# Kernel tuning notes

Hardware: AMD Instinct MI355X
Metric: run time of the kernel (lower is better)

Reference implementation:

```python
import jax, jax.numpy as jnp
import numpy as np

B, D, H, C, V, SAMPLE_NUM = 4096, 1024, 512, 50, 4, 10000


def ds_combin_two(alpha1, alpha2, K):
    """Dempster-Shafer combination of two Dirichlet parameter sets [B, K]."""
    S1 = jnp.sum(alpha1, axis=1, keepdims=True)
    S2 = jnp.sum(alpha2, axis=1, keepdims=True)
    b1 = (alpha1 - 1.0) / S1
    b2 = (alpha2 - 1.0) / S2
    u1 = K / S1  # [B,1]
    u2 = K / S2
    # bb_sum - bb_diag computed without materializing [B,K,K] outer product:
    # sum_ij b1_i b2_j = sum(b1)*sum(b2); diag sum = sum_i b1_i b2_i
    Cconf = jnp.sum(b1, axis=1) * jnp.sum(b2, axis=1) - jnp.sum(b1 * b2, axis=1)  # [B]
    denom = (1.0 - Cconf)[:, None]
    b_a = (b1 * b2 + b1 * u2 + b2 * u1) / denom
    u_a = (u1 * u2) / denom  # [B,1]
    S_a = K / u_a
    e_a = b_a * S_a
    return e_a + 1.0


def setup_inputs() -> dict:
    key = jax.random.key(0)
    ks = jax.random.split(key, 8)
    x = jax.random.normal(ks[0], (V, B, D), dtype=jnp.float32)
    indexes = jax.random.randint(ks[1], (B,), 0, SAMPLE_NUM)
    W1 = jax.random.normal(ks[2], (V, D, H), dtype=jnp.float32) * (1.0 / np.sqrt(D))
    b1 = jax.random.normal(ks[3], (V, H), dtype=jnp.float32) * 0.01
    W2 = jax.random.normal(ks[4], (V, H, C), dtype=jnp.float32) * (1.0 / np.sqrt(H))
    b2 = jax.random.normal(ks[5], (V, C), dtype=jnp.float32) * 0.01
    # original init: identity per (view, sample); add small noise so the
    eye = jnp.eye(C, dtype=jnp.float32)
    matrixes = eye[None, None] + 0.01 * jax.random.normal(ks[6], (V, SAMPLE_NUM, C, C), dtype=jnp.float32)
    return {"x": x, "indexes": indexes, "W1": W1, "b1": b1, "W2": W2, "b2": b2, "matrixes": matrixes}


def reference(x, indexes, W1, b1, W2, b2, matrixes):
    K = W2.shape[-1]
    n_views = x.shape[0]
    # per-view classifier MLP: Linear->ReLU->Linear->Softplus
    h = jax.nn.relu(jnp.einsum("vbd,vdh->vbh", x, W1) + b1[:, None, :])
    evidence = jax.nn.softplus(jnp.einsum("vbh,vhc->vbc", h, W2) + b2[:, None, :])  # [V,B,C]
    # transferByMatrix (training path): per-sample gathered [C,C] matmul
    sel = matrixes[:, indexes]  # [V,B,C,C]
    transferred = jnp.einsum("vbc,vbcd->vbd", evidence, sel)  # [V,B,C]
    t_alpha = transferred + 1.0
    # sequential DS combination over views
    alpha_a = t_alpha[0]
    for v in range(1, n_views):
        alpha_a = ds_combin_two(alpha_a, t_alpha[v], K)
    evidence_a = alpha_a - 1.0  # [B,C]
    return transferred, evidence_a, evidence
```

## Files before the change

kernel.cpp:

```cpp
#include <hip/hip_runtime.h>
#include <hip/hip_bf16.h>
#include <math.h>

typedef unsigned short u16;
typedef __attribute__((ext_vector_type(8))) short bf16x8;
typedef __attribute__((ext_vector_type(4))) float f32x4;

#define DEVI __device__ __forceinline__

constexpr int NV = 4;
constexpr int NB = 4096;
constexpr int ND = 1024;
constexpr int NH = 512;
constexpr int NC = 50;
constexpr int NSAMP = 10000;
constexpr int NCP = 64;

DEVI u16 to_bf16(float f) {
  union { float f; unsigned u; } v; v.f = f;
  unsigned r = v.u + 0x7fffu + ((v.u >> 16) & 1u);
  return (u16)(r >> 16);
}

DEVI u16 cvt_bf16(float f) {
  __hip_bfloat16 h = __float2bfloat16(f);
  return *reinterpret_cast<u16*>(&h);
}

DEVI float wsum(float x) {
#pragma unroll
  for (int m = 32; m > 0; m >>= 1) x += __shfl_xor(x, m, 64);
  return x;
}

#define GLD_LDS16(gsrc, ldst)                                                  \
  __builtin_amdgcn_global_load_lds(                                            \
      (const __attribute__((address_space(1))) void*)(gsrc),                   \
      (__attribute__((address_space(3))) void*)(ldst), 16, 0, 0)

__global__ __launch_bounds__(256) void k_transpose_w1(const float* __restrict__ W1,
                                                      u16* __restrict__ W1T) {
  __shared__ float tile[32][33];
  const int v = blockIdx.z;
  const int d0 = blockIdx.x * 32;
  const int h0 = blockIdx.y * 32;
  const float* src = W1 + (size_t)v * ND * NH;
  u16* dst = W1T + (size_t)v * NH * ND;
  const int tx = threadIdx.x, ty = threadIdx.y;
#pragma unroll
  for (int j = 0; j < 32; j += 8)
    tile[ty + j][tx] = src[(size_t)(d0 + ty + j) * NH + h0 + tx];
  __syncthreads();
#pragma unroll
  for (int j = 0; j < 32; j += 8)
    dst[(size_t)(h0 + ty + j) * ND + d0 + tx] = to_bf16(tile[tx][ty + j]);
}

__global__ __launch_bounds__(256) void k_prep_w2(const float* __restrict__ W2,
                                                 u16* __restrict__ W2T) {
  int i = blockIdx.x * blockDim.x + threadIdx.x;
  if (i >= NV * NCP * NH) return;
  int h = i % NH;
  int c = (i / NH) % NCP;
  int v = i / (NCP * NH);
  float val = (c < NC) ? W2[((size_t)v * NH + h) * NC + c] : 0.f;
  W2T[i] = to_bf16(val);
}

__global__ __launch_bounds__(256) void k_gemm1(const float* __restrict__ Xf,
                                               const u16* __restrict__ W1T,
                                               const float* __restrict__ b1,
                                               u16* __restrict__ Hb) {
  constexpr int BM = 128, BN = 128, BK = 32;
  const int v = blockIdx.z;
  const int m0 = blockIdx.x * BM;
  const int n0 = blockIdx.y * BN;
  __shared__ u16 As[BM][BK];
  __shared__ u16 Bs[BN][BK];
  const float* Ag = Xf + (size_t)v * NB * ND + (size_t)m0 * ND;
  const u16* Bg = W1T + (size_t)v * NH * ND + (size_t)n0 * ND;
  const int tid = threadIdx.x;
  const int lane = tid & 63;
  const int wv = tid >> 6;
  const int wr = wv >> 1, wc = wv & 1;
  const int rA = tid >> 3;
  const int cA = (tid & 7) * 4;
  const int rB = tid >> 2;
  const int cB = (tid & 3) * 8;

  f32x4 acc[4][4] = {};

  float4 pa[4];
#pragma unroll
  for (int i = 0; i < 4; ++i)
    pa[i] = *(const float4*)(Ag + (size_t)(rA + i * 32) * ND + cA);

  for (int k0 = 0; k0 < ND; k0 += BK) {
    __syncthreads();
#pragma unroll
    for (int i = 0; i < 4; ++i) {
      ushort4 u;
      u.x = cvt_bf16(pa[i].x); u.y = cvt_bf16(pa[i].y);
      u.z = cvt_bf16(pa[i].z); u.w = cvt_bf16(pa[i].w);
      *(ushort4*)&As[rA + i * 32][cA] = u;
    }
    GLD_LDS16(Bg + (size_t)rB * ND + k0 + cB,        &Bs[rB][cB]);
    GLD_LDS16(Bg + (size_t)(rB + 64) * ND + k0 + cB, &Bs[rB + 64][cB]);
    __syncthreads();

    if (k0 + BK < ND) {
#pragma unroll
      for (int i = 0; i < 4; ++i)
        pa[i] = *(const float4*)(Ag + (size_t)(rA + i * 32) * ND + k0 + BK + cA);
    }

    const int fr = lane & 15;
    const int kb = (lane >> 4) * 8;
    bf16x8 af[4], bf[4];
#pragma unroll
    for (int mi = 0; mi < 4; ++mi)
      af[mi] = *(const bf16x8*)&As[wr * 64 + mi * 16 + fr][kb];
#pragma unroll
    for (int ni = 0; ni < 4; ++ni)
      bf[ni] = *(const bf16x8*)&Bs[wc * 64 + ni * 16 + fr][kb];
#pragma unroll
    for (int mi = 0; mi < 4; ++mi)
#pragma unroll
      for (int ni = 0; ni < 4; ++ni)
        acc[mi][ni] = __builtin_amdgcn_mfma_f32_16x16x32_bf16(
            af[mi], bf[ni], acc[mi][ni], 0, 0, 0);
  }

  const int frow = (lane >> 4) * 4;
  const int fcol = lane & 15;
#pragma unroll
  for (int mi = 0; mi < 4; ++mi) {
#pragma unroll
    for (int ni = 0; ni < 4; ++ni) {
      const int n = n0 + wc * 64 + ni * 16 + fcol;
      const float bias = b1[v * NH + n];
#pragma unroll
      for (int j = 0; j < 4; ++j) {
        const int m = m0 + wr * 64 + mi * 16 + frow + j;
        float val = fmaxf(acc[mi][ni][j] + bias, 0.f);
        Hb[(size_t)v * NB * NH + (size_t)m * NH + n] = to_bf16(val);
      }
    }
  }
}

__global__ __launch_bounds__(256) void k_gemm2(const u16* __restrict__ Hb,
                                               const u16* __restrict__ W2T,
                                               const float* __restrict__ b2,
                                               float* __restrict__ out_ev) {
  constexpr int BM = 64, BK = 32;
  const int v = blockIdx.z;
  const int m0 = blockIdx.x * BM;
  __shared__ u16 As[BM][BK];
  __shared__ u16 Bs[NCP][BK];
  const u16* Ag = Hb + (size_t)v * NB * NH + (size_t)m0 * NH;
  const u16* Bg = W2T + (size_t)v * NCP * NH;
  const int tid = threadIdx.x;
  const int lane = tid & 63;
  const int wv = tid >> 6;
  const int r = tid >> 2;
  const int c8 = (tid & 3) * 8;

  f32x4 acc[4] = {};

  for (int k0 = 0; k0 < NH; k0 += BK) {
    __syncthreads();
    GLD_LDS16(Ag + (size_t)r * NH + k0 + c8, &As[r][c8]);
    GLD_LDS16(Bg + (size_t)r * NH + k0 + c8, &Bs[r][c8]);
    __syncthreads();

    const int fr = lane & 15;
    const int kb = (lane >> 4) * 8;
    bf16x8 af = *(const bf16x8*)&As[wv * 16 + fr][kb];
#pragma unroll
    for (int ni = 0; ni < 4; ++ni) {
      bf16x8 bf = *(const bf16x8*)&Bs[ni * 16 + fr][kb];
      acc[ni] = __builtin_amdgcn_mfma_f32_16x16x32_bf16(af, bf, acc[ni], 0, 0, 0);
    }
  }

  const int frow = (lane >> 4) * 4;
  const int fcol = lane & 15;
#pragma unroll
  for (int ni = 0; ni < 4; ++ni) {
    const int n = ni * 16 + fcol;
    if (n < NC) {
      const float bias = b2[v * NC + n];
#pragma unroll
      for (int j = 0; j < 4; ++j) {
        const int m = m0 + wv * 16 + frow + j;
        float x = acc[ni][j] + bias;
        float sp = fmaxf(x, 0.f) + log1pf(expf(-fabsf(x)));
        out_ev[(size_t)v * NB * NC + (size_t)m * NC + n] = sp;
      }
    }
  }
}

__global__ __launch_bounds__(256) void k_tc(const float* __restrict__ evf,
                                            const float* __restrict__ mats,
                                            const int* __restrict__ idx,
                                            float* __restrict__ out_tr,
                                            float* __restrict__ out_ea) {
  const int b = blockIdx.x * 4 + (threadIdx.x >> 6);
  const int lane = threadIdx.x & 63;
  if (b >= NB) return;
  const bool act = lane < NC;
  const float Kf = (float)NC;
  const int ix = idx[b];

  float ta[NV];
#pragma unroll
  for (int v = 0; v < NV; ++v) {
    float acc = 0.f;
    if (act) {
      const float* e = evf + ((size_t)v * NB + b) * NC;
      const float* M = mats + ((size_t)v * NSAMP + ix) * NC * NC;
#pragma unroll
      for (int c = 0; c < NC; ++c)
        acc = fmaf(e[c], M[c * NC + lane], acc);
      out_tr[((size_t)v * NB + b) * NC + lane] = acc;
    }
    ta[v] = act ? acc + 1.0f : 0.0f;
  }

  float alpha = ta[0];
#pragma unroll
  for (int v = 1; v < NV; ++v) {
    float a2 = ta[v];
    float S1 = wsum(act ? alpha : 0.f);
    float S2 = wsum(act ? a2 : 0.f);
    float b1v = act ? (alpha - 1.f) / S1 : 0.f;
    float b2v = act ? (a2 - 1.f) / S2 : 0.f;
    float u1 = Kf / S1, u2 = Kf / S2;
    float sb1 = wsum(b1v);
    float sb2 = wsum(b2v);
    float sb12 = wsum(b1v * b2v);
    float Cconf = sb1 * sb2 - sb12;
    float denom = 1.f - Cconf;
    float b_a = (b1v * b2v + b1v * u2 + b2v * u1) / denom;
    float u_a = u1 * u2 / denom;
    float S_a = Kf / u_a;
    alpha = b_a * S_a + 1.f;
  }
  if (act) out_ea[(size_t)b * NC + lane] = alpha - 1.f;
}

extern "C" void kernel_launch(void* const* d_in, const int* in_sizes, int n_in,
                              void* d_out, int out_size, void* d_ws, size_t ws_size,
                              hipStream_t stream) {
  const float *x = nullptr, *W1 = nullptr, *b1 = nullptr, *W2 = nullptr,
              *b2 = nullptr, *mats = nullptr;
  const int* idx = nullptr;
  for (int i = 0; i < n_in; ++i) {
    switch (in_sizes[i]) {
      case 16777216:  x    = (const float*)d_in[i]; break;
      case 4096:      idx  = (const int*)d_in[i];   break;
      case 2097152:   W1   = (const float*)d_in[i]; break;
      case 2048:      b1   = (const float*)d_in[i]; break;
      case 102400:    W2   = (const float*)d_in[i]; break;
      case 200:       b2   = (const float*)d_in[i]; break;
      case 100000000: mats = (const float*)d_in[i]; break;
      default: break;
    }
  }
  if (!x || !idx || !W1 || !b1 || !W2 || !b2 || !mats) return;

  char* ws = (char*)d_ws;
  u16* w1t = (u16*)(ws + 0);
  u16* w2t = (u16*)(ws + 4194304);
  u16* hb  = (u16*)(ws + 4456448);

  float* out_tr = (float*)d_out;
  float* out_ea = out_tr + (size_t)NV * NB * NC;
  float* out_ev = out_ea + (size_t)NB * NC;

  k_transpose_w1<<<dim3(ND / 32, NH / 32, NV), dim3(32, 8), 0, stream>>>(W1, w1t);
  k_prep_w2<<<(NV * NCP * NH + 255) / 256, 256, 0, stream>>>(W2, w2t);
  k_gemm1<<<dim3(NB / 128, NH / 128, NV), 256, 0, stream>>>(x, w1t, b1, hb);
  k_gemm2<<<dim3(NB / 64, 1, NV), 256, 0, stream>>>(hb, w2t, b2, out_ev);
  k_tc<<<NB / 4, 256, 0, stream>>>(out_ev, mats, idx, out_tr, out_ea);
}
```

Measured before the change: 92.36 us.

## Double gemm1 K-tile to 64 and merge weight prep kernels into one launch

The first GEMM now stages a 64-wide K slice per iteration instead of 32, doing two MFMA sub-steps per barrier pair and restructuring the A and B global-to-LDS load mapping. This halves the number of synchronisation rounds and loop overhead per tile. The W1 transpose and W2 padding kernels are fused into one launch using an extra grid row, removing a kernel launch. Larger prefetch register arrays and LDS usage may reduce occupancy, and the new LDS layout may add bank conflicts.

```diff
diff --git a/kernel.cpp b/kernel.cpp
--- a/kernel.cpp
+++ b/kernel.cpp
@@ -38,40 +38,43 @@
       (const __attribute__((address_space(1))) void*)(gsrc),                   \
       (__attribute__((address_space(3))) void*)(ldst), 16, 0, 0)
 
-__global__ __launch_bounds__(256) void k_transpose_w1(const float* __restrict__ W1,
-                                                      u16* __restrict__ W1T) {
+__global__ __launch_bounds__(256) void k_prep(const float* __restrict__ W1,
+                                              const float* __restrict__ W2,
+                                              u16* __restrict__ W1T,
+                                              u16* __restrict__ W2T) {
   __shared__ float tile[32][33];
   const int v = blockIdx.z;
-  const int d0 = blockIdx.x * 32;
-  const int h0 = blockIdx.y * 32;
-  const float* src = W1 + (size_t)v * ND * NH;
-  u16* dst = W1T + (size_t)v * NH * ND;
   const int tx = threadIdx.x, ty = threadIdx.y;
-#pragma unroll
-  for (int j = 0; j < 32; j += 8)
-    tile[ty + j][tx] = src[(size_t)(d0 + ty + j) * NH + h0 + tx];
-  __syncthreads();
-#pragma unroll
-  for (int j = 0; j < 32; j += 8)
-    dst[(size_t)(h0 + ty + j) * ND + d0 + tx] = to_bf16(tile[tx][ty + j]);
-}
-
-__global__ __launch_bounds__(256) void k_prep_w2(const float* __restrict__ W2,
-                                                 u16* __restrict__ W2T) {
-  int i = blockIdx.x * blockDim.x + threadIdx.x;
-  if (i >= NV * NCP * NH) return;
-  int h = i % NH;
-  int c = (i / NH) % NCP;
-  int v = i / (NCP * NH);
-  float val = (c < NC) ? W2[((size_t)v * NH + h) * NC + c] : 0.f;
-  W2T[i] = to_bf16(val);
+  if (blockIdx.y < NH / 32) {
+    const int d0 = blockIdx.x * 32;
+    const int h0 = blockIdx.y * 32;
+    const float* src = W1 + (size_t)v * ND * NH;
+    u16* dst = W1T + (size_t)v * NH * ND;
+#pragma unroll
+    for (int j = 0; j < 32; j += 8)
+      tile[ty + j][tx] = src[(size_t)(d0 + ty + j) * NH + h0 + tx];
+    __syncthreads();
+#pragma unroll
+    for (int j = 0; j < 32; j += 8)
+      dst[(size_t)(h0 + ty + j) * ND + d0 + tx] = to_bf16(tile[tx][ty + j]);
+  } else {
+    const int tid = ty * 32 + tx;
+#pragma unroll
+    for (int i = 0; i < 4; ++i) {
+      int e = blockIdx.x * 1024 + i * 256 + tid;
+      int h = e % NH;
+      int c = e / NH;
+      float val = (c < NC) ? W2[((size_t)v * NH + h) * NC + c] : 0.f;
+      W2T[(size_t)v * NCP * NH + e] = to_bf16(val);
+    }
+  }
 }
 
 __global__ __launch_bounds__(256) void k_gemm1(const float* __restrict__ Xf,
                                                const u16* __restrict__ W1T,
                                                const float* __restrict__ b1,
                                                u16* __restrict__ Hb) {
-  constexpr int BM = 128, BN = 128, BK = 32;
+  constexpr int BM = 128, BN = 128, BK = 64;
   const int v = blockIdx.z;
   const int m0 = blockIdx.x * BM;
   const int n0 = blockIdx.y * BN;
@@ -83,52 +86,58 @@
   const int lane = tid & 63;
   const int wv = tid >> 6;
   const int wr = wv >> 1, wc = wv & 1;
-  const int rA = tid >> 3;
-  const int cA = (tid & 7) * 4;
-  const int rB = tid >> 2;
-  const int cB = (tid & 3) * 8;
+  const int rA = tid >> 1;
+  const int cA = (tid & 1) * 32;
 
   f32x4 acc[4][4] = {};
 
-  float4 pa[4];
-#pragma unroll
-  for (int i = 0; i < 4; ++i)
-    pa[i] = *(const float4*)(Ag + (size_t)(rA + i * 32) * ND + cA);
+  float4 pa[8];
+#pragma unroll
+  for (int i = 0; i < 8; ++i)
+    pa[i] = *(const float4*)(Ag + (size_t)rA * ND + cA + i * 4);
 
   for (int k0 = 0; k0 < ND; k0 += BK) {
     __syncthreads();
 #pragma unroll
-    for (int i = 0; i < 4; ++i) {
+    for (int i = 0; i < 8; ++i) {
       ushort4 u;
       u.x = cvt_bf16(pa[i].x); u.y = cvt_bf16(pa[i].y);
       u.z = cvt_bf16(pa[i].z); u.w = cvt_bf16(pa[i].w);
-      *(ushort4*)&As[rA + i * 32][cA] = u;
-    }
-    GLD_LDS16(Bg + (size_t)rB * ND + k0 + cB,        &Bs[rB][cB]);
-    GLD_LDS16(Bg + (size_t)(rB + 64) * ND + k0 + cB, &Bs[rB + 64][cB]);
+      *(ushort4*)&As[rA][cA + i * 4] = u;
+    }
+#pragma unroll
+    for (int i = 0; i < 4; ++i) {
+      int s = tid + i * 256;
+      GLD_LDS16(Bg + (size_t)(s >> 3) * ND + k0 + (s & 7) * 8,
+                &Bs[s >> 3][(s & 7) * 8]);
+    }
     __syncthreads();
 
     if (k0 + BK < ND) {
 #pragma unroll
-      for (int i = 0; i < 4; ++i)
-        pa[i] = *(const float4*)(Ag + (size_t)(rA + i * 32) * ND + k0 + BK + cA);
+      for (int i = 0; i < 8; ++i)
+        pa[i] = *(const float4*)(Ag + (size_t)rA * ND + k0 + BK + cA + i * 4);
     }
 
     const int fr = lane & 15;
     const int kb = (lane >> 4) * 8;
-    bf16x8 af[4], bf[4];
-#pragma unroll
-    for (int mi = 0; mi < 4; ++mi)
-      af[mi] = *(const bf16x8*)&As[wr * 64 + mi * 16 + fr][kb];
-#pragma unroll
-    for (int ni = 0; ni < 4; ++ni)
-      bf[ni] = *(const bf16x8*)&Bs[wc * 64 + ni * 16 + fr][kb];
-#pragma unroll
-    for (int mi = 0; mi < 4; ++mi)
+#pragma unroll
+    for (int ks = 0; ks < 2; ++ks) {
+      const int ko = ks * 32 + kb;
+      bf16x8 af[4], bf[4];
+#pragma unroll
+      for (int mi = 0; mi < 4; ++mi)
+        af[mi] = *(const bf16x8*)&As[wr * 64 + mi * 16 + fr][ko];
 #pragma unroll
       for (int ni = 0; ni < 4; ++ni)
-        acc[mi][ni] = __builtin_amdgcn_mfma_f32_16x16x32_bf16(
-            af[mi], bf[ni], acc[mi][ni], 0, 0, 0);
+        bf[ni] = *(const bf16x8*)&Bs[wc * 64 + ni * 16 + fr][ko];
+#pragma unroll
+      for (int mi = 0; mi < 4; ++mi)
+#pragma unroll
+        for (int ni = 0; ni < 4; ++ni)
+          acc[mi][ni] = __builtin_amdgcn_mfma_f32_16x16x32_bf16(
+              af[mi], bf[ni], acc[mi][ni], 0, 0, 0);
+    }
   }
 
   const int frow = (lane >> 4) * 4;
@@ -280,8 +289,7 @@
   float* out_ea = out_tr + (size_t)NV * NB * NC;
   float* out_ev = out_ea + (size_t)NB * NC;
 
-  k_transpose_w1<<<dim3(ND / 32, NH / 32, NV), dim3(32, 8), 0, stream>>>(W1, w1t);
-  k_prep_w2<<<(NV * NCP * NH + 255) / 256, 256, 0, stream>>>(W2, w2t);
+  k_prep<<<dim3(32, NH / 32 + 1, NV), dim3(32, 8), 0, stream>>>(W1, W2, w1t, w2t);
   k_gemm1<<<dim3(NB / 128, NH / 128, NV), 256, 0, stream>>>(x, w1t, b1, hb);
   k_gemm2<<<dim3(NB / 64, 1, NV), 256, 0, stream>>>(hb, w2t, b2, out_ev);
   k_tc<<<NB / 4, 256, 0, stream>>>(out_ev, mats, idx, out_tr, out_ea);
```

New measurement: 100.8 us. 1.09x slower.
